# Kernel optimization log

Hardware: AMD Instinct MI355X
Metric: run time of the kernel (lower is better)

The kernel has to match this reference:

```python
import jax, jax.numpy as jnp
import numpy as np

B, N, E, H = 2, 512, 128, 256
IN_DIM = 3 * E + 1


def setup_inputs() -> dict:
    key = jax.random.key(0)
    ks = jax.random.split(key, 9)
    node_embed = jax.random.normal(ks[0], (B, N, E), dtype=jnp.float32)
    problems = jax.random.uniform(ks[1], (B, N, 4), dtype=jnp.float32)
    euclid = jax.random.uniform(ks[2], (B, N, N), dtype=jnp.float32)
    euclid = 0.5 * (euclid + jnp.swapaxes(euclid, 1, 2))  # symmetric, realistic
    s = 0.02
    W1 = s * jax.random.normal(ks[3], (IN_DIM, H), dtype=jnp.float32)
    b1 = jnp.zeros((H,), jnp.float32)
    W2 = s * jax.random.normal(ks[4], (H, H), dtype=jnp.float32)
    b2 = jnp.zeros((H,), jnp.float32)
    W3 = s * jax.random.normal(ks[5], (H, 1), dtype=jnp.float32)
    b3 = jnp.zeros((1,), jnp.float32)
    return {"node_embed": node_embed, "problems": problems,
            "euclid_distance_matrix": euclid,
            "W1": W1, "b1": b1, "W2": W2, "b2": b2, "W3": W3, "b3": b3}


def _forward(node_embed, euclid, W1, b1, W2, b2, W3, b3):
    b, n, e = node_embed.shape
    hi = jnp.broadcast_to(node_embed[:, :, None, :], (b, n, n, e))
    hj = jnp.broadcast_to(node_embed[:, None, :, :], (b, n, n, e))
    habs = jnp.abs(node_embed[:, :, None, :] - node_embed[:, None, :, :])
    x = jnp.concatenate([hi, hj, habs, euclid[..., None]], axis=-1)  # (B,N,N,3E+1)
    h = jax.nn.relu(jnp.einsum('bijf,fh->bijh', x, W1) + b1)
    h = jax.nn.relu(jnp.einsum('bijh,hg->bijg', h, W2) + b2)
    pred = (jnp.einsum('bijh,ho->bijo', h, W3) + b3)[..., 0]  # (B,N,N)
    pred = 0.5 * (pred + jnp.swapaxes(pred, 1, 2))
    pred = pred * (1.0 - jnp.eye(n, dtype=pred.dtype))  # zero diagonal
    return pred


def reference(node_embed, problems, euclid_distance_matrix, W1, b1, W2, b2, W3, b3):
    # euclid_distance_matrix provided, so `problems` fallback path is unused
    return _forward(node_embed, euclid_distance_matrix, W1, b1, W2, b2, W3, b3)
```

## Files before the change

kernel.cpp:

```cpp
#include <hip/hip_runtime.h>
#include <hip/hip_bf16.h>


#define BN 512
#define EE 128
#define HH 256

typedef __attribute__((ext_vector_type(8)))  short short8;
typedef __attribute__((ext_vector_type(16))) float f32x16;
typedef __attribute__((ext_vector_type(4)))  float f32x4;

static __device__ __forceinline__ unsigned short f2bf(float f) {
    __bf16 h = (__bf16)f;
    return __builtin_bit_cast(unsigned short, h);
}
static __device__ __forceinline__ float bf2f(unsigned short s) {
    return (float)__builtin_bit_cast(__bf16, s);
}
static __device__ __forceinline__ f32x16 zero16() {
    f32x16 v;
    #pragma unroll
    for (int i = 0; i < 16; ++i) v[i] = 0.f;
    return v;
}
#define MFMA(a, b, c) __builtin_amdgcn_mfma_f32_32x32x16_bf16((a), (b), (c), 0, 0, 0)

__global__ void prep(const float* __restrict__ node, const float* __restrict__ W1,
                     const float* __restrict__ W2, const float* __restrict__ b1,
                     const float* __restrict__ b2, float* __restrict__ PA,
                     unsigned short* __restrict__ w1c_p, unsigned short* __restrict__ w1b_p,
                     unsigned short* __restrict__ w2_p,  unsigned short* __restrict__ w1d_f,
                     unsigned short* __restrict__ b2_f,  unsigned short* __restrict__ node_p) {
    int blk = blockIdx.x;
    if (blk < 512) {
        int idx = blk * 256 + threadIdx.x;
        {
            int t = idx & 7, l = (idx >> 3) & 63, kb = (idx >> 9) & 7;
            int j32 = (idx >> 12) & 15, b = (idx >> 16) & 1;
            int j = j32 * 32 + (l & 31), e = kb * 16 + (l >> 5) * 8 + t;
            node_p[idx] = f2bf(node[((size_t)b * BN + j) * EE + e]);
        }
        if (idx < 65536) {
            int t = idx & 7, l = (idx >> 3) & 63, nb = (idx >> 9) & 7, kb = idx >> 12;
            int k = kb * 16 + (l >> 5) * 8 + t, n = nb * 32 + (l & 31);
            w2_p[idx] = f2bf(W2[k * HH + n]);
            if (idx < 32768) {
                w1c_p[idx] = f2bf(W1[(2 * EE + k) * HH + n]);
                w1b_p[idx] = f2bf(W1[(EE + k) * HH + n]);
            }
        }
        if (idx < 4096) {
            int t = idx & 7, l = (idx >> 3) & 63, nb = idx >> 9;
            int n = nb * 32 + (l & 31);
            bool nz = (t == 0 && l < 32);
            w1d_f[idx] = nz ? f2bf(W1[(3 * EE) * HH + n]) : (unsigned short)0;
            b2_f[idx]  = nz ? f2bf(b2[n]) : (unsigned short)0;
        }
    } else {
        int bi = blk - 512;
        int h = threadIdx.x;
        const float* nd = node + (size_t)bi * EE;
        float sa = b1[h];
        #pragma unroll 8
        for (int e = 0; e < EE; ++e) sa += nd[e] * W1[e * HH + h];
        PA[bi * HH + h] = sa;
    }
}

__global__ __launch_bounds__(256, 2) void edge_main(
    const float* __restrict__ node, const float* __restrict__ euclid,
    const float* __restrict__ W3, const float* __restrict__ b3,
    const float* __restrict__ PA,
    const unsigned short* __restrict__ w1c_p, const unsigned short* __restrict__ w1b_p,
    const unsigned short* __restrict__ w2_p,  const unsigned short* __restrict__ w1d_f,
    const unsigned short* __restrict__ b2_f,  const unsigned short* __restrict__ node_p,
    float* __restrict__ out)
{
    __shared__ __align__(16) unsigned short lds_buf[128 * 264];
    __shared__ float pp[256];

    const int jt = blockIdx.x, i = blockIdx.y, b = blockIdx.z;
    const int jbase = jt * 128;
    const int tid = threadIdx.x, wave = tid >> 6, lane = tid & 63;
    const int m0 = lane & 31, q = lane >> 5, kq = q * 8;
    const int col0 = wave * 64 + m0;

    {
        int row = tid >> 1, half = tid & 1;
        const f32x4* nj = (const f32x4*)(node + ((size_t)b * BN + jbase + row) * EE);
        const f32x4* hv = (const f32x4*)(node + ((size_t)b * BN + i) * EE);
        unsigned short* dst = &lds_buf[row * 136 + half * 64];
        #pragma unroll
        for (int g = 0; g < 8; ++g) {
            int c0 = half * 16 + g * 2;
            f32x4 a0 = nj[c0], a1 = nj[c0 + 1];
            f32x4 h0 = hv[c0], h1v = hv[c0 + 1];
            short8 pd;
            #pragma unroll
            for (int u = 0; u < 4; ++u) {
                pd[u]     = (short)f2bf(fabsf(a0[u] - h0[u]));
                pd[4 + u] = (short)f2bf(fabsf(a1[u] - h1v[u]));
            }
            *(short8*)(dst + g * 8) = pd;
        }
    }
    __syncthreads();

    f32x16 acc[4][2];
    #pragma unroll
    for (int mt = 0; mt < 4; ++mt) { acc[mt][0] = zero16(); acc[mt][1] = zero16(); }
    {
        const short8* bc = (const short8*)w1c_p;
        const short8* bb = (const short8*)w1b_p;
        const short8* np = (const short8*)node_p;
        const int npb = b * 128 + jt * 32;
        #pragma unroll
        for (int kb = 0; kb < 8; ++kb) {
            short8 b0 = bc[(kb * 8 + wave * 2 + 0) * 64 + lane];
            short8 b1 = bc[(kb * 8 + wave * 2 + 1) * 64 + lane];
            short8 c0 = bb[(kb * 8 + wave * 2 + 0) * 64 + lane];
            short8 c1 = bb[(kb * 8 + wave * 2 + 1) * 64 + lane];
            #pragma unroll
            for (int mt = 0; mt < 4; ++mt) {
                short8 ad = *(const short8*)&lds_buf[(mt * 32 + m0) * 136 + kb * 16 + kq];
                short8 ah = np[(npb + mt * 8 + kb) * 64 + lane];
                acc[mt][0] = MFMA(ad, b0, acc[mt][0]);
                acc[mt][1] = MFMA(ad, b1, acc[mt][1]);
                acc[mt][0] = MFMA(ah, c0, acc[mt][0]);
                acc[mt][1] = MFMA(ah, c1, acc[mt][1]);
            }
        }
        const float* erow = euclid + ((size_t)b * BN + i) * BN + jbase;
        short8 d0 = ((const short8*)w1d_f)[(wave * 2 + 0) * 64 + lane];
        short8 d1 = ((const short8*)w1d_f)[(wave * 2 + 1) * 64 + lane];
        #pragma unroll
        for (int mt = 0; mt < 4; ++mt) {
            short8 ae;
            #pragma unroll
            for (int u = 0; u < 8; ++u) ae[u] = 0;
            if (lane < 32) ae[0] = (short)f2bf(erow[mt * 32 + m0]);
            acc[mt][0] = MFMA(ae, d0, acc[mt][0]);
            acc[mt][1] = MFMA(ae, d1, acc[mt][1]);
        }
    }
    __syncthreads();

    {
        const float* paRow = PA + ((size_t)b * BN + i) * HH;
        float pa0 = paRow[col0], pa1 = paRow[col0 + 32];
        int rq = 4 * q;
        #pragma unroll
        for (int mt = 0; mt < 4; ++mt) {
            #pragma unroll
            for (int r = 0; r < 16; ++r) {
                int row = mt * 32 + (r & 3) + 8 * (r >> 2) + rq;
                float v0 = acc[mt][0][r] + pa0; v0 = v0 > 0.f ? v0 : 0.f;
                float v1 = acc[mt][1][r] + pa1; v1 = v1 > 0.f ? v1 : 0.f;
                lds_buf[row * 264 + col0]      = f2bf(v0);
                lds_buf[row * 264 + col0 + 32] = f2bf(v1);
            }
        }
    }
    __syncthreads();

    f32x16 c2[4][2];
    #pragma unroll
    for (int mt = 0; mt < 4; ++mt) { c2[mt][0] = zero16(); c2[mt][1] = zero16(); }
    {
        const short8* bp = (const short8*)w2_p;
        #pragma unroll
        for (int kb = 0; kb < 16; ++kb) {
            short8 b0 = bp[(kb * 8 + wave * 2 + 0) * 64 + lane];
            short8 b1 = bp[(kb * 8 + wave * 2 + 1) * 64 + lane];
            #pragma unroll
            for (int mt = 0; mt < 4; ++mt) {
                short8 a = *(const short8*)&lds_buf[(mt * 32 + m0) * 264 + kb * 16 + kq];
                c2[mt][0] = MFMA(a, b0, c2[mt][0]);
                c2[mt][1] = MFMA(a, b1, c2[mt][1]);
            }
        }
        short8 aone;
        #pragma unroll
        for (int u = 0; u < 8; ++u) aone[u] = 0;
        if (lane < 32) aone[0] = (short)0x3F80;
        short8 e0 = ((const short8*)b2_f)[(wave * 2 + 0) * 64 + lane];
        short8 e1 = ((const short8*)b2_f)[(wave * 2 + 1) * 64 + lane];
        #pragma unroll
        for (int mt = 0; mt < 4; ++mt) {
            c2[mt][0] = MFMA(aone, e0, c2[mt][0]);
            c2[mt][1] = MFMA(aone, e1, c2[mt][1]);
        }
    }
    __syncthreads();

    {
        int rq = 4 * q;
        #pragma unroll
        for (int mt = 0; mt < 4; ++mt) {
            #pragma unroll
            for (int r = 0; r < 16; ++r) {
                int row = mt * 32 + (r & 3) + 8 * (r >> 2) + rq;
                float v0 = c2[mt][0][r] > 0.f ? c2[mt][0][r] : 0.f;
                float v1 = c2[mt][1][r] > 0.f ? c2[mt][1][r] : 0.f;
                lds_buf[row * 264 + col0]      = f2bf(v0);
                lds_buf[row * 264 + col0 + 32] = f2bf(v1);
            }
        }
    }
    __syncthreads();

    {
        int row = tid >> 1, halfc = (tid & 1) * 128;
        float s = 0.f;
        #pragma unroll
        for (int k = 0; k < 16; ++k) {
            short8 h8 = *(const short8*)&lds_buf[row * 264 + halfc + k * 8];
            #pragma unroll
            for (int u = 0; u < 8; ++u)
                s += bf2f((unsigned short)h8[u]) * W3[halfc + k * 8 + u];
        }
        pp[tid] = s;
    }
    __syncthreads();
    if (tid < 128) {
        float v = pp[tid * 2] + pp[tid * 2 + 1] + b3[0];
        out[((size_t)b * BN + i) * BN + jbase + tid] = v;
    }
}

__global__ void symmetrize(float* __restrict__ out) {
    int b = blockIdx.z, ti = blockIdx.y, tj = blockIdx.x;
    if (tj < ti) return;
    int i = ti * 32 + threadIdx.y, j = tj * 32 + threadIdx.x;
    float* p = out + (size_t)b * BN * BN;
    if (i == j) { p[(size_t)i * BN + j] = 0.f; return; }
    if (j < i) return;
    float a = p[(size_t)i * BN + j];
    float c = p[(size_t)j * BN + i];
    float v = 0.5f * (a + c);
    p[(size_t)i * BN + j] = v;
    p[(size_t)j * BN + i] = v;
}

extern "C" void kernel_launch(void* const* d_in, const int* in_sizes, int n_in,
                              void* d_out, int out_size, void* d_ws, size_t ws_size,
                              hipStream_t stream) {
    const float* node   = (const float*)d_in[0];
    const float* euclid = (const float*)d_in[2];
    const float* W1     = (const float*)d_in[3];
    const float* b1     = (const float*)d_in[4];
    const float* W2     = (const float*)d_in[5];
    const float* b2     = (const float*)d_in[6];
    const float* W3     = (const float*)d_in[7];
    const float* b3     = (const float*)d_in[8];
    float* out = (float*)d_out;

    char* ws = (char*)d_ws;
    float*          PA     = (float*)ws;
    unsigned short* w1c_p  = (unsigned short*)(ws + (1u << 20));
    unsigned short* w1b_p  = (unsigned short*)(ws + (1u << 20) + 65536);
    unsigned short* w2_p   = (unsigned short*)(ws + (1u << 20) + 131072);
    unsigned short* w1d_f  = (unsigned short*)(ws + (1u << 20) + 262144);
    unsigned short* b2_f   = (unsigned short*)(ws + (1u << 20) + 270336);
    unsigned short* node_p = (unsigned short*)(ws + (1u << 20) + 278528);

    prep<<<1536, 256, 0, stream>>>(node, W1, W2, b1, b2, PA,
                                   w1c_p, w1b_p, w2_p, w1d_f, b2_f, node_p);
    edge_main<<<dim3(BN / 128, BN, 2), 256, 0, stream>>>(
        node, euclid, W3, b3, PA, w1c_p, w1b_p, w2_p, w1d_f, b2_f, node_p, out);
    symmetrize<<<dim3(BN / 32, BN / 32, 2), dim3(32, 32), 0, stream>>>(out);
}
```

Baseline: 268.3 us.

## Transpose MFMA roles so layer-2 output feeds W3 dot in registers

Swaps the MFMA operand roles so weights are the A operand and the edge features (from LDS) are the B operand, making hidden features lie along the row dimension of each accumulator. This allows the layer-2 bias, ReLU and W3 dot product to be computed directly from registers with a cross-half shuffle, removing the second LDS write-back, one barrier and the bias MFMA. Node_j features are now converted into LDS in-kernel instead of a pre-packed global copy, shrinking the prep kernel. It adds a second LDS tile and a vectorized layer-1 store pattern, with possible changes in bank conflicts.

```diff
diff --git a/kernel.cpp b/kernel.cpp
--- a/kernel.cpp
+++ b/kernel.cpp
@@ -7,15 +7,13 @@
 #define HH 256
 
 typedef __attribute__((ext_vector_type(8)))  short short8;
+typedef __attribute__((ext_vector_type(4)))  short short4v;
 typedef __attribute__((ext_vector_type(16))) float f32x16;
 typedef __attribute__((ext_vector_type(4)))  float f32x4;
 
 static __device__ __forceinline__ unsigned short f2bf(float f) {
     __bf16 h = (__bf16)f;
     return __builtin_bit_cast(unsigned short, h);
-}
-static __device__ __forceinline__ float bf2f(unsigned short s) {
-    return (float)__builtin_bit_cast(__bf16, s);
 }
 static __device__ __forceinline__ f32x16 zero16() {
     f32x16 v;
@@ -27,37 +25,29 @@
 
 __global__ void prep(const float* __restrict__ node, const float* __restrict__ W1,
                      const float* __restrict__ W2, const float* __restrict__ b1,
-                     const float* __restrict__ b2, float* __restrict__ PA,
+                     float* __restrict__ PA,
                      unsigned short* __restrict__ w1c_p, unsigned short* __restrict__ w1b_p,
-                     unsigned short* __restrict__ w2_p,  unsigned short* __restrict__ w1d_f,
-                     unsigned short* __restrict__ b2_f,  unsigned short* __restrict__ node_p) {
+                     unsigned short* __restrict__ w2_p,  unsigned short* __restrict__ w1d_f) {
     int blk = blockIdx.x;
-    if (blk < 512) {
+    if (blk < 256) {
         int idx = blk * 256 + threadIdx.x;
         {
-            int t = idx & 7, l = (idx >> 3) & 63, kb = (idx >> 9) & 7;
-            int j32 = (idx >> 12) & 15, b = (idx >> 16) & 1;
-            int j = j32 * 32 + (l & 31), e = kb * 16 + (l >> 5) * 8 + t;
-            node_p[idx] = f2bf(node[((size_t)b * BN + j) * EE + e]);
-        }
-        if (idx < 65536) {
-            int t = idx & 7, l = (idx >> 3) & 63, nb = (idx >> 9) & 7, kb = idx >> 12;
-            int k = kb * 16 + (l >> 5) * 8 + t, n = nb * 32 + (l & 31);
-            w2_p[idx] = f2bf(W2[k * HH + n]);
+            int t = idx & 7, l = (idx >> 3) & 63, mt = (idx >> 9) & 7, kb = idx >> 12;
+            int k = kb * 16 + (l >> 5) * 8 + t, m = mt * 32 + (l & 31);
+            w2_p[idx] = f2bf(W2[k * HH + m]);
             if (idx < 32768) {
-                w1c_p[idx] = f2bf(W1[(2 * EE + k) * HH + n]);
-                w1b_p[idx] = f2bf(W1[(EE + k) * HH + n]);
+                w1c_p[idx] = f2bf(W1[(2 * EE + k) * HH + m]);
+                w1b_p[idx] = f2bf(W1[(EE + k) * HH + m]);
             }
         }
         if (idx < 4096) {
-            int t = idx & 7, l = (idx >> 3) & 63, nb = idx >> 9;
-            int n = nb * 32 + (l & 31);
+            int t = idx & 7, l = (idx >> 3) & 63, mt = idx >> 9;
+            int m = mt * 32 + (l & 31);
             bool nz = (t == 0 && l < 32);
-            w1d_f[idx] = nz ? f2bf(W1[(3 * EE) * HH + n]) : (unsigned short)0;
-            b2_f[idx]  = nz ? f2bf(b2[n]) : (unsigned short)0;
+            w1d_f[idx] = nz ? f2bf(W1[(3 * EE) * HH + m]) : (unsigned short)0;
         }
     } else {
-        int bi = blk - 512;
+        int bi = blk - 256;
         int h = threadIdx.x;
         const float* nd = node + (size_t)bi * EE;
         float sa = b1[h];
@@ -70,160 +60,173 @@
 __global__ __launch_bounds__(256, 2) void edge_main(
     const float* __restrict__ node, const float* __restrict__ euclid,
     const float* __restrict__ W3, const float* __restrict__ b3,
-    const float* __restrict__ PA,
+    const float* __restrict__ b2v, const float* __restrict__ PA,
     const unsigned short* __restrict__ w1c_p, const unsigned short* __restrict__ w1b_p,
     const unsigned short* __restrict__ w2_p,  const unsigned short* __restrict__ w1d_f,
-    const unsigned short* __restrict__ b2_f,  const unsigned short* __restrict__ node_p,
     float* __restrict__ out)
 {
-    __shared__ __align__(16) unsigned short lds_buf[128 * 264];
-    __shared__ float pp[256];
+    __shared__ __align__(16) unsigned short lds_buf[2 * 128 * 136];
+    __shared__ float pp[512];
 
     const int jt = blockIdx.x, i = blockIdx.y, b = blockIdx.z;
     const int jbase = jt * 128;
     const int tid = threadIdx.x, wave = tid >> 6, lane = tid & 63;
-    const int m0 = lane & 31, q = lane >> 5, kq = q * 8;
-    const int col0 = wave * 64 + m0;
+    const int m0 = lane & 31, q = lane >> 5;
+
+    unsigned short* ldsD  = lds_buf;
+    unsigned short* ldsHJ = lds_buf + 128 * 136;
+    unsigned short* ldsH1 = lds_buf;
 
     {
         int row = tid >> 1, half = tid & 1;
         const f32x4* nj = (const f32x4*)(node + ((size_t)b * BN + jbase + row) * EE);
         const f32x4* hv = (const f32x4*)(node + ((size_t)b * BN + i) * EE);
-        unsigned short* dst = &lds_buf[row * 136 + half * 64];
         #pragma unroll
         for (int g = 0; g < 8; ++g) {
             int c0 = half * 16 + g * 2;
             f32x4 a0 = nj[c0], a1 = nj[c0 + 1];
             f32x4 h0 = hv[c0], h1v = hv[c0 + 1];
-            short8 pd;
+            short8 pd, ph;
             #pragma unroll
             for (int u = 0; u < 4; ++u) {
                 pd[u]     = (short)f2bf(fabsf(a0[u] - h0[u]));
                 pd[4 + u] = (short)f2bf(fabsf(a1[u] - h1v[u]));
-            }
-            *(short8*)(dst + g * 8) = pd;
-        }
-    }
-    __syncthreads();
-
-    f32x16 acc[4][2];
+                ph[u]     = (short)f2bf(a0[u]);
+                ph[4 + u] = (short)f2bf(a1[u]);
+            }
+            int off = row * 136 + half * 64 + g * 8;
+            *(short8*)&ldsD[off]  = pd;
+            *(short8*)&ldsHJ[off] = ph;
+        }
+    }
+    __syncthreads();
+
+    f32x16 acc[2][4];
     #pragma unroll
-    for (int mt = 0; mt < 4; ++mt) { acc[mt][0] = zero16(); acc[mt][1] = zero16(); }
-    {
-        const short8* bc = (const short8*)w1c_p;
-        const short8* bb = (const short8*)w1b_p;
-        const short8* np = (const short8*)node_p;
-        const int npb = b * 128 + jt * 32;
+    for (int mt = 0; mt < 2; ++mt)
+        #pragma unroll
+        for (int nt = 0; nt < 4; ++nt) acc[mt][nt] = zero16();
+    {
+        const short8* wc = (const short8*)w1c_p;
+        const short8* wb = (const short8*)w1b_p;
+        const int mtg = wave * 2;
         #pragma unroll
         for (int kb = 0; kb < 8; ++kb) {
-            short8 b0 = bc[(kb * 8 + wave * 2 + 0) * 64 + lane];
-            short8 b1 = bc[(kb * 8 + wave * 2 + 1) * 64 + lane];
-            short8 c0 = bb[(kb * 8 + wave * 2 + 0) * 64 + lane];
-            short8 c1 = bb[(kb * 8 + wave * 2 + 1) * 64 + lane];
-            #pragma unroll
-            for (int mt = 0; mt < 4; ++mt) {
-                short8 ad = *(const short8*)&lds_buf[(mt * 32 + m0) * 136 + kb * 16 + kq];
-                short8 ah = np[(npb + mt * 8 + kb) * 64 + lane];
-                acc[mt][0] = MFMA(ad, b0, acc[mt][0]);
-                acc[mt][1] = MFMA(ad, b1, acc[mt][1]);
-                acc[mt][0] = MFMA(ah, c0, acc[mt][0]);
-                acc[mt][1] = MFMA(ah, c1, acc[mt][1]);
+            short8 ac0 = wc[(kb * 8 + mtg + 0) * 64 + lane];
+            short8 ac1 = wc[(kb * 8 + mtg + 1) * 64 + lane];
+            short8 ab0 = wb[(kb * 8 + mtg + 0) * 64 + lane];
+            short8 ab1 = wb[(kb * 8 + mtg + 1) * 64 + lane];
+            #pragma unroll
+            for (int nt = 0; nt < 4; ++nt) {
+                int off = (nt * 32 + m0) * 136 + kb * 16 + q * 8;
+                short8 bD  = *(const short8*)&ldsD[off];
+                short8 bHJ = *(const short8*)&ldsHJ[off];
+                acc[0][nt] = MFMA(ac0, bD, acc[0][nt]);
+                acc[1][nt] = MFMA(ac1, bD, acc[1][nt]);
+                acc[0][nt] = MFMA(ab0, bHJ, acc[0][nt]);
+                acc[1][nt] = MFMA(ab1, bHJ, acc[1][nt]);
             }
         }
         const float* erow = euclid + ((size_t)b * BN + i) * BN + jbase;
-        short8 d0 = ((const short8*)w1d_f)[(wave * 2 + 0) * 64 + lane];
-        short8 d1 = ((const short8*)w1d_f)[(wave * 2 + 1) * 64 + lane];
-        #pragma unroll
-        for (int mt = 0; mt < 4; ++mt) {
-            short8 ae;
-            #pragma unroll
-            for (int u = 0; u < 8; ++u) ae[u] = 0;
-            if (lane < 32) ae[0] = (short)f2bf(erow[mt * 32 + m0]);
-            acc[mt][0] = MFMA(ae, d0, acc[mt][0]);
-            acc[mt][1] = MFMA(ae, d1, acc[mt][1]);
-        }
-    }
-    __syncthreads();
-
-    {
-        const float* paRow = PA + ((size_t)b * BN + i) * HH;
-        float pa0 = paRow[col0], pa1 = paRow[col0 + 32];
-        int rq = 4 * q;
-        #pragma unroll
-        for (int mt = 0; mt < 4; ++mt) {
-            #pragma unroll
-            for (int r = 0; r < 16; ++r) {
-                int row = mt * 32 + (r & 3) + 8 * (r >> 2) + rq;
-                float v0 = acc[mt][0][r] + pa0; v0 = v0 > 0.f ? v0 : 0.f;
-                float v1 = acc[mt][1][r] + pa1; v1 = v1 > 0.f ? v1 : 0.f;
-                lds_buf[row * 264 + col0]      = f2bf(v0);
-                lds_buf[row * 264 + col0 + 32] = f2bf(v1);
-            }
-        }
-    }
-    __syncthreads();
-
-    f32x16 c2[4][2];
+        short8 aw0 = ((const short8*)w1d_f)[(mtg + 0) * 64 + lane];
+        short8 aw1 = ((const short8*)w1d_f)[(mtg + 1) * 64 + lane];
+        #pragma unroll
+        for (int nt = 0; nt < 4; ++nt) {
+            short8 be;
+            #pragma unroll
+            for (int u = 0; u < 8; ++u) be[u] = 0;
+            if (lane < 32) be[0] = (short)f2bf(erow[nt * 32 + m0]);
+            acc[0][nt] = MFMA(aw0, be, acc[0][nt]);
+            acc[1][nt] = MFMA(aw1, be, acc[1][nt]);
+        }
+    }
+    __syncthreads();
+
+    {
+        const float* paB = PA + ((size_t)b * BN + i) * HH;
+        #pragma unroll
+        for (int mt = 0; mt < 2; ++mt) {
+            #pragma unroll
+            for (int rg = 0; rg < 4; ++rg) {
+                int f0 = wave * 64 + mt * 32 + rg * 8;
+                f32x4 plo = *(const f32x4*)&paB[f0];
+                f32x4 phi = *(const f32x4*)&paB[f0 + 4];
+                f32x4 pav;
+                #pragma unroll
+                for (int u = 0; u < 4; ++u) pav[u] = q ? phi[u] : plo[u];
+                #pragma unroll
+                for (int nt = 0; nt < 4; ++nt) {
+                    short4v w;
+                    #pragma unroll
+                    for (int u = 0; u < 4; ++u) {
+                        float v = acc[mt][nt][rg * 4 + u] + pav[u];
+                        v = v > 0.f ? v : 0.f;
+                        w[u] = (short)f2bf(v);
+                    }
+                    *(short4v*)&ldsH1[(nt * 32 + m0) * 264 + f0 + 4 * q] = w;
+                }
+            }
+        }
+    }
+    __syncthreads();
+
+    f32x16 c2[2][4];
     #pragma unroll
-    for (int mt = 0; mt < 4; ++mt) { c2[mt][0] = zero16(); c2[mt][1] = zero16(); }
-    {
-        const short8* bp = (const short8*)w2_p;
+    for (int mt = 0; mt < 2; ++mt)
+        #pragma unroll
+        for (int nt = 0; nt < 4; ++nt) c2[mt][nt] = zero16();
+    {
+        const short8* w2f = (const short8*)w2_p;
+        const int mtg = wave * 2;
         #pragma unroll
         for (int kb = 0; kb < 16; ++kb) {
-            short8 b0 = bp[(kb * 8 + wave * 2 + 0) * 64 + lane];
-            short8 b1 = bp[(kb * 8 + wave * 2 + 1) * 64 + lane];
-            #pragma unroll
-            for (int mt = 0; mt < 4; ++mt) {
-                short8 a = *(const short8*)&lds_buf[(mt * 32 + m0) * 264 + kb * 16 + kq];
-                c2[mt][0] = MFMA(a, b0, c2[mt][0]);
-                c2[mt][1] = MFMA(a, b1, c2[mt][1]);
-            }
-        }
-        short8 aone;
-        #pragma unroll
-        for (int u = 0; u < 8; ++u) aone[u] = 0;
-        if (lane < 32) aone[0] = (short)0x3F80;
-        short8 e0 = ((const short8*)b2_f)[(wave * 2 + 0) * 64 + lane];
-        short8 e1 = ((const short8*)b2_f)[(wave * 2 + 1) * 64 + lane];
-        #pragma unroll
-        for (int mt = 0; mt < 4; ++mt) {
-            c2[mt][0] = MFMA(aone, e0, c2[mt][0]);
-            c2[mt][1] = MFMA(aone, e1, c2[mt][1]);
-        }
-    }
-    __syncthreads();
-
-    {
-        int rq = 4 * q;
-        #pragma unroll
-        for (int mt = 0; mt < 4; ++mt) {
-            #pragma unroll
-            for (int r = 0; r < 16; ++r) {
-                int row = mt * 32 + (r & 3) + 8 * (r >> 2) + rq;
-                float v0 = c2[mt][0][r] > 0.f ? c2[mt][0][r] : 0.f;
-                float v1 = c2[mt][1][r] > 0.f ? c2[mt][1][r] : 0.f;
-                lds_buf[row * 264 + col0]      = f2bf(v0);
-                lds_buf[row * 264 + col0 + 32] = f2bf(v1);
-            }
-        }
-    }
-    __syncthreads();
-
-    {
-        int row = tid >> 1, halfc = (tid & 1) * 128;
-        float s = 0.f;
-        #pragma unroll
-        for (int k = 0; k < 16; ++k) {
-            short8 h8 = *(const short8*)&lds_buf[row * 264 + halfc + k * 8];
-            #pragma unroll
-            for (int u = 0; u < 8; ++u)
-                s += bf2f((unsigned short)h8[u]) * W3[halfc + k * 8 + u];
-        }
-        pp[tid] = s;
+            short8 a0 = w2f[(kb * 8 + mtg + 0) * 64 + lane];
+            short8 a1 = w2f[(kb * 8 + mtg + 1) * 64 + lane];
+            #pragma unroll
+            for (int nt = 0; nt < 4; ++nt) {
+                short8 bh = *(const short8*)&ldsH1[(nt * 32 + m0) * 264 + kb * 16 + q * 8];
+                c2[0][nt] = MFMA(a0, bh, c2[0][nt]);
+                c2[1][nt] = MFMA(a1, bh, c2[1][nt]);
+            }
+        }
+    }
+
+    {
+        float s[4] = {0.f, 0.f, 0.f, 0.f};
+        #pragma unroll
+        for (int mt = 0; mt < 2; ++mt) {
+            #pragma unroll
+            for (int rg = 0; rg < 4; ++rg) {
+                int f0 = wave * 64 + mt * 32 + rg * 8;
+                f32x4 blo = *(const f32x4*)&b2v[f0];
+                f32x4 bhi = *(const f32x4*)&b2v[f0 + 4];
+                f32x4 wlo = *(const f32x4*)&W3[f0];
+                f32x4 whi = *(const f32x4*)&W3[f0 + 4];
+                #pragma unroll
+                for (int u = 0; u < 4; ++u) {
+                    float bb = q ? bhi[u] : blo[u];
+                    float ww = q ? whi[u] : wlo[u];
+                    #pragma unroll
+                    for (int nt = 0; nt < 4; ++nt) {
+                        float h2 = c2[mt][nt][rg * 4 + u] + bb;
+                        h2 = h2 > 0.f ? h2 : 0.f;
+                        s[nt] += h2 * ww;
+                    }
+                }
+            }
+        }
+        #pragma unroll
+        for (int nt = 0; nt < 4; ++nt)
+            s[nt] += __shfl_xor(s[nt], 32, 64);
+        if (lane < 32) {
+            #pragma unroll
+            for (int nt = 0; nt < 4; ++nt)
+                pp[wave * 128 + nt * 32 + lane] = s[nt];
+        }
     }
     __syncthreads();
     if (tid < 128) {
-        float v = pp[tid * 2] + pp[tid * 2 + 1] + b3[0];
+        float v = pp[tid] + pp[128 + tid] + pp[256 + tid] + pp[384 + tid] + b3[0];
         out[((size_t)b * BN + i) * BN + jbase + tid] = v;
     }
 }
@@ -256,17 +259,14 @@
     float* out = (float*)d_out;
 
     char* ws = (char*)d_ws;
-    float*          PA     = (float*)ws;
-    unsigned short* w1c_p  = (unsigned short*)(ws + (1u << 20));
-    unsigned short* w1b_p  = (unsigned short*)(ws + (1u << 20) + 65536);
-    unsigned short* w2_p   = (unsigned short*)(ws + (1u << 20) + 131072);
-    unsigned short* w1d_f  = (unsigned short*)(ws + (1u << 20) + 262144);
-    unsigned short* b2_f   = (unsigned short*)(ws + (1u << 20) + 270336);
-    unsigned short* node_p = (unsigned short*)(ws + (1u << 20) + 278528);
-
-    prep<<<1536, 256, 0, stream>>>(node, W1, W2, b1, b2, PA,
-                                   w1c_p, w1b_p, w2_p, w1d_f, b2_f, node_p);
+    float*          PA    = (float*)ws;
+    unsigned short* w1c_p = (unsigned short*)(ws + (1u << 20));
+    unsigned short* w1b_p = (unsigned short*)(ws + (1u << 20) + 65536);
+    unsigned short* w2_p  = (unsigned short*)(ws + (1u << 20) + 131072);
+    unsigned short* w1d_f = (unsigned short*)(ws + (1u << 20) + 262144);
+
+    prep<<<1280, 256, 0, stream>>>(node, W1, W2, b1, PA, w1c_p, w1b_p, w2_p, w1d_f);
     edge_main<<<dim3(BN / 128, BN, 2), 256, 0, stream>>>(
-        node, euclid, W3, b3, PA, w1c_p, w1b_p, w2_p, w1d_f, b2_f, node_p, out);
+        node, euclid, W3, b3, b2, PA, w1c_p, w1b_p, w2_p, w1d_f, out);
     symmetrize<<<dim3(BN / 32, BN / 32, 2), dim3(32, 32), 0, stream>>>(out);
 }
```

Result: faster. 236.1 us (-12.0%).
